# Optimization experiments

Measured on AMD Instinct MI355X. Metric: run time of the kernel, lower is better.

Reference implementation:

```python
import jax, jax.numpy as jnp
import numpy as np

TOP_K = 8
N_GROUPS = 8
TOP_K_GROUPS = 4
ROUTE_SCALE = 2.5


def setup_inputs() -> dict:
    key = jax.random.key(0)
    k1, k2, k3 = jax.random.split(key, 3)
    x = jax.random.normal(k1, (8192, 7168), dtype=jnp.float32)
    weight = jax.random.normal(k2, (256, 7168), dtype=jnp.float32) * 0.02
    bias = jax.random.normal(k3, (256,), dtype=jnp.float32) * 0.1
    return {"x": x, "weight": weight, "bias": bias}


def reference(x, weight, bias):
    n_tokens = x.shape[0]
    n_experts = weight.shape[0]
    # scores: [T, E]
    logits = jnp.einsum('td,ed->te', x, weight)
    scores = jax.nn.sigmoid(logits)
    original_scores = scores
    scores_b = scores + bias  # bias branch (dim == 7168)
    # group-limited routing
    sg = scores_b.reshape(n_tokens, N_GROUPS, n_experts // N_GROUPS)
    # bias is not None -> group score = sum of top-2 within group
    top2, _ = jax.lax.top_k(sg, 2)
    group_scores = top2.sum(axis=-1)  # [T, G]
    _, group_idx = jax.lax.top_k(group_scores, TOP_K_GROUPS)  # [T, Kg]
    keep = jnp.zeros((n_tokens, N_GROUPS), dtype=bool)
    keep = keep.at[jnp.arange(n_tokens)[:, None], group_idx].set(True)
    masked = jnp.where(keep[:, :, None], sg, -jnp.inf).reshape(n_tokens, n_experts)
    # global top-k over masked scores
    _, indices = jax.lax.top_k(masked, TOP_K)  # [T, K]
    weights = jnp.take_along_axis(original_scores, indices, axis=1)
    weights = weights / weights.sum(axis=-1, keepdims=True)  # sigmoid normalization
    weights = weights * ROUTE_SCALE
    return weights.astype(x.dtype), indices
```

## Files before the change

### kernel.cpp

```cpp
#include <hip/hip_runtime.h>
#include <math.h>

#define T_TOKENS 8192
#define NEXP 256
#define DIM 7168
#define NEG_INF (-3.0e38f)

typedef _Float16 f16;
typedef _Float16 f16x8 __attribute__((ext_vector_type(8)));
typedef __fp16 h16x2 __attribute__((ext_vector_type(2)));
typedef float f32x4 __attribute__((ext_vector_type(4)));

#define AS1 __attribute__((address_space(1)))
#define AS3 __attribute__((address_space(3)))

#define WPLANE_BYTES (NEXP * DIM * 2)
#define PART_OFF (2 * WPLANE_BYTES)
#define UNSCALE 5.9604644775390625e-8f

__global__ __launch_bounds__(256) void wconvert(const float* __restrict__ w,
                                                f16* __restrict__ w0p,
                                                f16* __restrict__ w1p) {
    const int i = (blockIdx.x * 256 + threadIdx.x) * 8;
    const f32x4 u0 = *(const f32x4*)(w + i);
    const f32x4 u1 = *(const f32x4*)(w + i + 4);
    float c[8] = {u0[0]*4096.f, u0[1]*4096.f, u0[2]*4096.f, u0[3]*4096.f,
                  u1[0]*4096.f, u1[1]*4096.f, u1[2]*4096.f, u1[3]*4096.f};
    f16x8 h, g;
#pragma unroll
    for (int j = 0; j < 4; ++j) {
        h16x2 hp = __builtin_amdgcn_cvt_pkrtz(c[2*j], c[2*j+1]);
        float r0 = c[2*j]   - (float)hp[0];
        float r1 = c[2*j+1] - (float)hp[1];
        h16x2 gp = __builtin_amdgcn_cvt_pkrtz(r0, r1);
        h[2*j] = (f16)hp[0]; h[2*j+1] = (f16)hp[1];
        g[2*j] = (f16)gp[0]; g[2*j+1] = (f16)gp[1];
    }
    *(f16x8*)(w0p + i) = h;
    *(f16x8*)(w1p + i) = g;
}

__global__ __launch_bounds__(256, 2) void gemm_f16split_db(
    const float* __restrict__ x, const f16* __restrict__ w0,
    float* __restrict__ part, int ksplit) {
    __shared__ char smem[65536];
    const int tid = threadIdx.x;
    const int lane = tid & 63;
    const int wv = tid >> 6;
    const int bm = blockIdx.x, bn = blockIdx.y, bz = blockIdx.z;
    const int wr = wv >> 1, wc = wv & 1;
    const int l15 = lane & 15, q4 = lane >> 4;

    const char* xc = (const char*)x;
    const char* wcp = (const char*)w0;

    int aoff[4], woff[4], ldsA[4], ldsW[4];
#pragma unroll
    for (int i = 0; i < 4; ++i) {
        const int ai = wv * 4 + i;
        const int ra = ai * 8 + (lane >> 3);
        const int ua = lane & 7;
        aoff[i] = (bm * 128 + ra) * (DIM * 4) + bz * (ksplit * 4)
                + ((ua ^ (ra & 7)) * 16);
        ldsA[i] = ai * 1024;
        const int wi_ = wv * 4 + i;
        const int p = wi_ >> 3;
        const int rw = (wi_ & 7) * 16 + (lane >> 2);
        const int uw = lane & 3;
        woff[i] = p * WPLANE_BYTES + (bn * 128 + rw) * (DIM * 2) + bz * (ksplit * 2)
                + ((uw ^ ((rw >> 1) & 3)) * 16);
        ldsW[i] = 16384 + wi_ * 1024;
    }

    int rA[4][2], rW[4][2];
#pragma unroll
    for (int m = 0; m < 4; ++m) {
        const int r = wr * 64 + m * 16 + l15;
        rA[m][0] = r * 128 + (((2 * q4 + 0) ^ (r & 7)) * 16);
        rA[m][1] = r * 128 + (((2 * q4 + 1) ^ (r & 7)) * 16);
    }
#pragma unroll
    for (int n = 0; n < 4; ++n) {
        const int rw = wc * 64 + n * 16 + l15;
        rW[n][0] = 16384 + 0    + rw * 64 + ((q4 ^ ((rw >> 1) & 3)) * 16);
        rW[n][1] = 16384 + 8192 + rw * 64 + ((q4 ^ ((rw >> 1) & 3)) * 16);
    }

    f32x4 acc[4][4];
#pragma unroll
    for (int m = 0; m < 4; ++m)
#pragma unroll
        for (int n = 0; n < 4; ++n) acc[m][n] = (f32x4){0.f, 0.f, 0.f, 0.f};

#define STAGE(sb)                                                               \
    {                                                                           \
        _Pragma("unroll")                                                       \
        for (int i = 0; i < 4; ++i)                                             \
            __builtin_amdgcn_global_load_lds((const AS1 void*)(xc + aoff[i]),   \
                (AS3 void*)(smem + (sb) + ldsA[i]), 16, 0, 0);                  \
        _Pragma("unroll")                                                       \
        for (int i = 0; i < 4; ++i)                                             \
            __builtin_amdgcn_global_load_lds((const AS1 void*)(wcp + woff[i]),  \
                (AS3 void*)(smem + (sb) + ldsW[i]), 16, 0, 0);                  \
        _Pragma("unroll")                                                       \
        for (int i = 0; i < 4; ++i) { aoff[i] += 128; woff[i] += 64; }          \
    }

#define COMPUTE(sb)                                                             \
    {                                                                           \
        f16x8 bfr[4][2];                                                        \
        _Pragma("unroll")                                                       \
        for (int n = 0; n < 4; ++n) {                                           \
            bfr[n][0] = *(const f16x8*)(smem + (sb) + rW[n][0]);                \
            bfr[n][1] = *(const f16x8*)(smem + (sb) + rW[n][1]);                \
        }                                                                       \
        _Pragma("unroll")                                                       \
        for (int m = 0; m < 4; ++m) {                                           \
            const f32x4 v0 = *(const f32x4*)(smem + (sb) + rA[m][0]);           \
            const f32x4 v1 = *(const f32x4*)(smem + (sb) + rA[m][1]);           \
            float c[8] = {v0[0]*4096.f, v0[1]*4096.f, v0[2]*4096.f, v0[3]*4096.f,\
                          v1[0]*4096.f, v1[1]*4096.f, v1[2]*4096.f, v1[3]*4096.f};\
            f16x8 a0, a1;                                                       \
            _Pragma("unroll")                                                   \
            for (int j = 0; j < 4; ++j) {                                       \
                h16x2 hp = __builtin_amdgcn_cvt_pkrtz(c[2*j], c[2*j+1]);        \
                float r0 = c[2*j]   - (float)hp[0];                             \
                float r1 = c[2*j+1] - (float)hp[1];                             \
                h16x2 gp = __builtin_amdgcn_cvt_pkrtz(r0, r1);                  \
                a0[2*j] = (f16)hp[0]; a0[2*j+1] = (f16)hp[1];                   \
                a1[2*j] = (f16)gp[0]; a1[2*j+1] = (f16)gp[1];                   \
            }                                                                   \
            __builtin_amdgcn_s_setprio(1);                                      \
            _Pragma("unroll")                                                   \
            for (int n = 0; n < 4; ++n) {                                       \
                acc[m][n] = __builtin_amdgcn_mfma_f32_16x16x32_f16(a0, bfr[n][0], acc[m][n], 0, 0, 0); \
                acc[m][n] = __builtin_amdgcn_mfma_f32_16x16x32_f16(a1, bfr[n][0], acc[m][n], 0, 0, 0); \
                acc[m][n] = __builtin_amdgcn_mfma_f32_16x16x32_f16(a0, bfr[n][1], acc[m][n], 0, 0, 0); \
                acc[m][n] = __builtin_amdgcn_mfma_f32_16x16x32_f16(a1, bfr[n][1], acc[m][n], 0, 0, 0); \
            }                                                                   \
            __builtin_amdgcn_s_setprio(0);                                      \
        }                                                                       \
    }

    const int niter = ksplit >> 5;
    STAGE(0);
    for (int t = 0; t < niter - 1; ++t) {
        const int cur = (t & 1) * 32768;
        const int nxt = ((t + 1) & 1) * 32768;
        STAGE(nxt);
        asm volatile("s_waitcnt vmcnt(8)" ::: "memory");
        __builtin_amdgcn_sched_barrier(0);
        __builtin_amdgcn_s_barrier();
        COMPUTE(cur);
        __builtin_amdgcn_s_barrier();
    }
    asm volatile("s_waitcnt vmcnt(0)" ::: "memory");
    __builtin_amdgcn_sched_barrier(0);
    __builtin_amdgcn_s_barrier();
    COMPUTE(((niter - 1) & 1) * 32768);
#undef STAGE
#undef COMPUTE

    float* P = part + (size_t)bz * T_TOKENS * NEXP;
    const int orow = bm * 128 + wr * 64 + (lane >> 4) * 4;
    const int ocol = bn * 128 + wc * 64 + l15;
#pragma unroll
    for (int m = 0; m < 4; ++m)
#pragma unroll
        for (int n = 0; n < 4; ++n)
#pragma unroll
            for (int r = 0; r < 4; ++r)
                P[(size_t)(orow + m * 16 + r) * NEXP + ocol + n * 16] = acc[m][n][r];
}

__global__ __launch_bounds__(256) void routing_kernel(const float* __restrict__ part,
                                                      const float* __restrict__ bias,
                                                      float* __restrict__ out, int nsplit) {
    const int lane = threadIdx.x & 63;
    const int t = blockIdx.x * 4 + (threadIdx.x >> 6);

    f32x4 z = {0.f, 0.f, 0.f, 0.f};
    for (int s = 0; s < nsplit; ++s) {
        const f32x4 v = *((const f32x4*)(part + ((size_t)s * T_TOKENS + t) * NEXP) + lane);
        z[0] += v[0]; z[1] += v[1]; z[2] += v[2]; z[3] += v[3];
    }
    const float s0 = 1.0f / (1.0f + expf(-z[0] * UNSCALE));
    const float s1 = 1.0f / (1.0f + expf(-z[1] * UNSCALE));
    const float s2 = 1.0f / (1.0f + expf(-z[2] * UNSCALE));
    const float s3 = 1.0f / (1.0f + expf(-z[3] * UNSCALE));
    const f32x4 bv = *((const f32x4*)bias + lane);
    float sb0 = s0 + bv[0], sb1 = s1 + bv[1], sb2 = s2 + bv[2], sb3 = s3 + bv[3];

    float m1, m2;
    m1 = sb0; m2 = NEG_INF;
    if (sb1 > m1) { m2 = m1; m1 = sb1; } else if (sb1 > m2) m2 = sb1;
    if (sb2 > m1) { m2 = m1; m1 = sb2; } else if (sb2 > m2) m2 = sb2;
    if (sb3 > m1) { m2 = m1; m1 = sb3; } else if (sb3 > m2) m2 = sb3;
#pragma unroll
    for (int off = 1; off < 8; off <<= 1) {
        const float om1 = __shfl_xor(m1, off);
        const float om2 = __shfl_xor(m2, off);
        const float hi = fmaxf(m1, om1);
        const float lo = fminf(m1, om1);
        m2 = fmaxf(lo, fmaxf(m2, om2));
        m1 = hi;
    }
    const float gs = m1 + m2;

    const float g0 = __shfl(gs, 0),  g1 = __shfl(gs, 8),  g2 = __shfl(gs, 16), g3 = __shfl(gs, 24);
    const float g4 = __shfl(gs, 32), g5 = __shfl(gs, 40), g6 = __shfl(gs, 48), g7 = __shfl(gs, 56);

    float t1 = NEG_INF, t2 = NEG_INF, t3 = NEG_INF, t4 = NEG_INF;
    int i1 = 0, i2 = 0, i3 = 0, i4 = 0;
#define INS4(v, gi)                                                         \
    {                                                                       \
        if (v > t1)      { t4=t3;i4=i3; t3=t2;i3=i2; t2=t1;i2=i1; t1=v;i1=gi; } \
        else if (v > t2) { t4=t3;i4=i3; t3=t2;i3=i2; t2=v;i2=gi; }          \
        else if (v > t3) { t4=t3;i4=i3; t3=v;i3=gi; }                       \
        else if (v > t4) { t4=v;i4=gi; }                                    \
    }
    INS4(g0, 0) INS4(g1, 1) INS4(g2, 2) INS4(g3, 3)
    INS4(g4, 4) INS4(g5, 5) INS4(g6, 6) INS4(g7, 7)
#undef INS4
    const int keepmask = (1 << i1) | (1 << i2) | (1 << i3) | (1 << i4);

    const int g = lane >> 3;
    if (!((keepmask >> g) & 1)) { sb0 = NEG_INF; sb1 = NEG_INF; sb2 = NEG_INF; sb3 = NEG_INF; }

    float wval[8];
    int wi[8];
    float wsum = 0.0f;
#pragma unroll
    for (int r = 0; r < 8; r++) {
        float bvv = sb0;
        int bii = (lane << 2);
        if (sb1 > bvv) { bvv = sb1; bii = (lane << 2) | 1; }
        if (sb2 > bvv) { bvv = sb2; bii = (lane << 2) | 2; }
        if (sb3 > bvv) { bvv = sb3; bii = (lane << 2) | 3; }
#pragma unroll
        for (int off = 1; off < 64; off <<= 1) {
            const float ov = __shfl_xor(bvv, off);
            const int oi = __shfl_xor(bii, off);
            if (ov > bvv || (ov == bvv && oi < bii)) { bvv = ov; bii = oi; }
        }
        const int sl = bii & 3;
        const float cand = (sl == 0) ? s0 : (sl == 1) ? s1 : (sl == 2) ? s2 : s3;
        const float ow = __shfl(cand, bii >> 2);
        wval[r] = ow;
        wi[r] = bii;
        wsum += ow;
        if ((bii >> 2) == lane) {
            if (sl == 0) sb0 = NEG_INF;
            else if (sl == 1) sb1 = NEG_INF;
            else if (sl == 2) sb2 = NEG_INF;
            else sb3 = NEG_INF;
        }
    }
    const float scale = 2.5f / wsum;
    if (lane == 0) {
        float* ow8 = out + (size_t)t * 8;
        float* oi8 = out + (size_t)T_TOKENS * 8 + (size_t)t * 8;
#pragma unroll
        for (int r = 0; r < 8; r++) {
            ow8[r] = wval[r] * scale;
            oi8[r] = (float)wi[r];
        }
    }
}

extern "C" void kernel_launch(void* const* d_in, const int* in_sizes, int n_in,
                              void* d_out, int out_size, void* d_ws, size_t ws_size,
                              hipStream_t stream) {
    const float* x = (const float*)d_in[0];
    const float* w = (const float*)d_in[1];
    const float* bias = (const float*)d_in[2];

    f16* w0 = (f16*)d_ws;
    f16* w1 = (f16*)((char*)d_ws + WPLANE_BYTES);
    float* part = (float*)((char*)d_ws + PART_OFF);

    const size_t need4 = (size_t)PART_OFF + 4ull * T_TOKENS * NEXP * 4;
    const int nsplit = (ws_size >= need4) ? 4 : 2;
    const int ksplit = DIM / nsplit;

    wconvert<<<NEXP * DIM / (256 * 8), 256, 0, stream>>>(w, w0, w1);
    gemm_f16split_db<<<dim3(64, 2, nsplit), 256, 0, stream>>>(x, w0, part, ksplit);
    routing_kernel<<<T_TOKENS / 4, 256, 0, stream>>>(part, bias, (float*)d_out, nsplit);
}
```

Measured before the change: 141.5 us.

## Rewrite router GEMM with 32x32 MFMA, pre-tiled weights and register-loaded activations

The weight-conversion kernel now writes the split-f16 weights in a pre-tiled layout that matches the MFMA operand order, so the GEMM can stage W into LDS with plain contiguous copies. Activations are loaded straight into registers instead of through LDS, which halves shared memory use. The MFMA is switched from 16x16x32 to 32x32x16, and the grid is reordered so the two N-blocks sharing an M tile are adjacent. The aim is less LDS traffic and fewer instructions per MFMA, in exchange for more register pressure, direct global loads of x, and a more involved software pipeline.

```diff
diff --git a/kernel.cpp b/kernel.cpp
--- a/kernel.cpp
+++ b/kernel.cpp
@@ -10,20 +10,22 @@
 typedef _Float16 f16x8 __attribute__((ext_vector_type(8)));
 typedef __fp16 h16x2 __attribute__((ext_vector_type(2)));
 typedef float f32x4 __attribute__((ext_vector_type(4)));
+typedef float f32x16 __attribute__((ext_vector_type(16)));
 
 #define AS1 __attribute__((address_space(1)))
 #define AS3 __attribute__((address_space(3)))
 
-#define WPLANE_BYTES (NEXP * DIM * 2)
-#define PART_OFF (2 * WPLANE_BYTES)
+#define WTILED_BYTES (2 * NEXP * DIM * 2)
+#define PART_OFF WTILED_BYTES
 #define UNSCALE 5.9604644775390625e-8f
 
 __global__ __launch_bounds__(256) void wconvert(const float* __restrict__ w,
-                                                f16* __restrict__ w0p,
-                                                f16* __restrict__ w1p) {
-    const int i = (blockIdx.x * 256 + threadIdx.x) * 8;
-    const f32x4 u0 = *(const f32x4*)(w + i);
-    const f32x4 u1 = *(const f32x4*)(w + i + 4);
+                                                char* __restrict__ wt) {
+    const int n = blockIdx.x * 256 + threadIdx.x;
+    const int K8 = n % 896;
+    const int eg = n / 896;
+    const f32x4 u0 = *(const f32x4*)(w + eg * DIM + K8 * 8);
+    const f32x4 u1 = *(const f32x4*)(w + eg * DIM + K8 * 8 + 4);
     float c[8] = {u0[0]*4096.f, u0[1]*4096.f, u0[2]*4096.f, u0[3]*4096.f,
                   u1[0]*4096.f, u1[1]*4096.f, u1[2]*4096.f, u1[3]*4096.f};
     f16x8 h, g;
@@ -36,141 +38,162 @@
         h[2*j] = (f16)hp[0]; h[2*j+1] = (f16)hp[1];
         g[2*j] = (f16)gp[0]; g[2*j+1] = (f16)gp[1];
     }
-    *(f16x8*)(w0p + i) = h;
-    *(f16x8*)(w1p + i) = g;
+    const int T = K8 >> 2, ksub = (K8 >> 1) & 1, kch = K8 & 1;
+    const int bn = eg >> 7, E = eg & 127, np_ = E >> 5, e = E & 31;
+    const int base = (T * 2 + bn) * 16384 + kch * 512 + e * 16;
+    *(f16x8*)(wt + base + ((ksub * 2 + 0) * 4 + np_) * 1024) = h;
+    *(f16x8*)(wt + base + ((ksub * 2 + 1) * 4 + np_) * 1024) = g;
 }
 
-__global__ __launch_bounds__(256, 2) void gemm_f16split_db(
-    const float* __restrict__ x, const f16* __restrict__ w0,
+__global__ __launch_bounds__(256) void gemm32(
+    const float* __restrict__ x, const char* __restrict__ wt,
     float* __restrict__ part, int ksplit) {
-    __shared__ char smem[65536];
+    __shared__ char smem[32768];
     const int tid = threadIdx.x;
     const int lane = tid & 63;
     const int wv = tid >> 6;
-    const int bm = blockIdx.x, bn = blockIdx.y, bz = blockIdx.z;
-    const int wr = wv >> 1, wc = wv & 1;
-    const int l15 = lane & 15, q4 = lane >> 4;
-
-    const char* xc = (const char*)x;
-    const char* wcp = (const char*)w0;
-
-    int aoff[4], woff[4], ldsA[4], ldsW[4];
-#pragma unroll
-    for (int i = 0; i < 4; ++i) {
-        const int ai = wv * 4 + i;
-        const int ra = ai * 8 + (lane >> 3);
-        const int ua = lane & 7;
-        aoff[i] = (bm * 128 + ra) * (DIM * 4) + bz * (ksplit * 4)
-                + ((ua ^ (ra & 7)) * 16);
-        ldsA[i] = ai * 1024;
-        const int wi_ = wv * 4 + i;
-        const int p = wi_ >> 3;
-        const int rw = (wi_ & 7) * 16 + (lane >> 2);
-        const int uw = lane & 3;
-        woff[i] = p * WPLANE_BYTES + (bn * 128 + rw) * (DIM * 2) + bz * (ksplit * 2)
-                + ((uw ^ ((rw >> 1) & 3)) * 16);
-        ldsW[i] = 16384 + wi_ * 1024;
-    }
-
-    int rA[4][2], rW[4][2];
-#pragma unroll
-    for (int m = 0; m < 4; ++m) {
-        const int r = wr * 64 + m * 16 + l15;
-        rA[m][0] = r * 128 + (((2 * q4 + 0) ^ (r & 7)) * 16);
-        rA[m][1] = r * 128 + (((2 * q4 + 1) ^ (r & 7)) * 16);
-    }
-#pragma unroll
-    for (int n = 0; n < 4; ++n) {
-        const int rw = wc * 64 + n * 16 + l15;
-        rW[n][0] = 16384 + 0    + rw * 64 + ((q4 ^ ((rw >> 1) & 3)) * 16);
-        rW[n][1] = 16384 + 8192 + rw * 64 + ((q4 ^ ((rw >> 1) & 3)) * 16);
-    }
-
-    f32x4 acc[4][4];
-#pragma unroll
-    for (int m = 0; m < 4; ++m)
-#pragma unroll
-        for (int n = 0; n < 4; ++n) acc[m][n] = (f32x4){0.f, 0.f, 0.f, 0.f};
-
-#define STAGE(sb)                                                               \
+    const int bn = blockIdx.x, bm = blockIdx.y, bz = blockIdx.z;
+    const int wr = wv >> 1, wcn = wv & 1;
+    const int l31 = lane & 31, lhi = lane >> 5;
+
+    const float* arow[2];
+#pragma unroll
+    for (int mp = 0; mp < 2; ++mp)
+        arow[mp] = x + (size_t)(bm * 128 + wr * 64 + mp * 32 + l31) * DIM
+                 + bz * ksplit + lhi * 8;
+
+    const int niter = ksplit >> 5;
+    const char* wsrc = wt + (size_t)(bz * niter * 2 + bn) * 16384 + (wv * 4) * 1024 + lane * 16;
+    const int ldsw = (wv * 4) * 1024;
+
+    int rW[2][2][2];
+#pragma unroll
+    for (int ks = 0; ks < 2; ++ks)
+#pragma unroll
+        for (int p = 0; p < 2; ++p)
+#pragma unroll
+            for (int np_ = 0; np_ < 2; ++np_)
+                rW[ks][p][np_] = ((ks * 2 + p) * 4 + (wcn * 2 + np_)) * 1024
+                               + lhi * 512 + l31 * 16;
+
+    f32x16 acc[2][2];
+#pragma unroll
+    for (int mp = 0; mp < 2; ++mp)
+#pragma unroll
+        for (int np_ = 0; np_ < 2; ++np_)
+#pragma unroll
+            for (int r = 0; r < 16; ++r) acc[mp][np_][r] = 0.0f;
+
+    f32x4 ab[2][2][2];
+
+#define LOAD_A(koff)                                                            \
     {                                                                           \
         _Pragma("unroll")                                                       \
-        for (int i = 0; i < 4; ++i)                                             \
-            __builtin_amdgcn_global_load_lds((const AS1 void*)(xc + aoff[i]),   \
-                (AS3 void*)(smem + (sb) + ldsA[i]), 16, 0, 0);                  \
+        for (int mp = 0; mp < 2; ++mp)                                          \
+            _Pragma("unroll")                                                   \
+            for (int ks = 0; ks < 2; ++ks) {                                    \
+                ab[mp][ks][0] = *(const f32x4*)(arow[mp] + (koff) + ks * 16);   \
+                ab[mp][ks][1] = *(const f32x4*)(arow[mp] + (koff) + ks * 16 + 4);\
+            }                                                                   \
+    }
+
+#define STAGE_W(t, sb)                                                          \
+    {                                                                           \
+        const char* s_ = wsrc + (size_t)(t) * 32768;                            \
         _Pragma("unroll")                                                       \
         for (int i = 0; i < 4; ++i)                                             \
-            __builtin_amdgcn_global_load_lds((const AS1 void*)(wcp + woff[i]),  \
-                (AS3 void*)(smem + (sb) + ldsW[i]), 16, 0, 0);                  \
+            __builtin_amdgcn_global_load_lds((const AS1 void*)(s_ + i * 1024),  \
+                (AS3 void*)(smem + (sb) + ldsw + i * 1024), 16, 0, 0);          \
+    }
+
+#define CONVERT()                                                               \
+    f16x8 fa0[2][2], fa1[2][2];                                                 \
+    {                                                                           \
         _Pragma("unroll")                                                       \
-        for (int i = 0; i < 4; ++i) { aoff[i] += 128; woff[i] += 64; }          \
-    }
-
-#define COMPUTE(sb)                                                             \
+        for (int mp = 0; mp < 2; ++mp)                                          \
+            _Pragma("unroll")                                                   \
+            for (int ks = 0; ks < 2; ++ks) {                                    \
+                float c[8] = {ab[mp][ks][0][0]*4096.f, ab[mp][ks][0][1]*4096.f, \
+                              ab[mp][ks][0][2]*4096.f, ab[mp][ks][0][3]*4096.f, \
+                              ab[mp][ks][1][0]*4096.f, ab[mp][ks][1][1]*4096.f, \
+                              ab[mp][ks][1][2]*4096.f, ab[mp][ks][1][3]*4096.f};\
+                _Pragma("unroll")                                               \
+                for (int j = 0; j < 4; ++j) {                                   \
+                    h16x2 hp = __builtin_amdgcn_cvt_pkrtz(c[2*j], c[2*j+1]);    \
+                    float r0 = c[2*j]   - (float)hp[0];                         \
+                    float r1 = c[2*j+1] - (float)hp[1];                         \
+                    h16x2 gp = __builtin_amdgcn_cvt_pkrtz(r0, r1);              \
+                    fa0[mp][ks][2*j] = (f16)hp[0]; fa0[mp][ks][2*j+1] = (f16)hp[1]; \
+                    fa1[mp][ks][2*j] = (f16)gp[0]; fa1[mp][ks][2*j+1] = (f16)gp[1]; \
+                }                                                               \
+            }                                                                   \
+    }
+
+#define MFMA_STEP(sb)                                                           \
     {                                                                           \
-        f16x8 bfr[4][2];                                                        \
+        __builtin_amdgcn_s_setprio(1);                                          \
         _Pragma("unroll")                                                       \
-        for (int n = 0; n < 4; ++n) {                                           \
-            bfr[n][0] = *(const f16x8*)(smem + (sb) + rW[n][0]);                \
-            bfr[n][1] = *(const f16x8*)(smem + (sb) + rW[n][1]);                \
-        }                                                                       \
-        _Pragma("unroll")                                                       \
-        for (int m = 0; m < 4; ++m) {                                           \
-            const f32x4 v0 = *(const f32x4*)(smem + (sb) + rA[m][0]);           \
-            const f32x4 v1 = *(const f32x4*)(smem + (sb) + rA[m][1]);           \
-            float c[8] = {v0[0]*4096.f, v0[1]*4096.f, v0[2]*4096.f, v0[3]*4096.f,\
-                          v1[0]*4096.f, v1[1]*4096.f, v1[2]*4096.f, v1[3]*4096.f};\
-            f16x8 a0, a1;                                                       \
+        for (int ks = 0; ks < 2; ++ks)                                          \
             _Pragma("unroll")                                                   \
-            for (int j = 0; j < 4; ++j) {                                       \
-                h16x2 hp = __builtin_amdgcn_cvt_pkrtz(c[2*j], c[2*j+1]);        \
-                float r0 = c[2*j]   - (float)hp[0];                             \
-                float r1 = c[2*j+1] - (float)hp[1];                             \
-                h16x2 gp = __builtin_amdgcn_cvt_pkrtz(r0, r1);                  \
-                a0[2*j] = (f16)hp[0]; a0[2*j+1] = (f16)hp[1];                   \
-                a1[2*j] = (f16)gp[0]; a1[2*j+1] = (f16)gp[1];                   \
+            for (int np_ = 0; np_ < 2; ++np_) {                                 \
+                const f16x8 wb0 = *(const f16x8*)(smem + (sb) + rW[ks][0][np_]);\
+                const f16x8 wb1 = *(const f16x8*)(smem + (sb) + rW[ks][1][np_]);\
+                _Pragma("unroll")                                               \
+                for (int mp = 0; mp < 2; ++mp) {                                \
+                    acc[mp][np_] = __builtin_amdgcn_mfma_f32_32x32x16_f16(fa0[mp][ks], wb0, acc[mp][np_], 0, 0, 0); \
+                    acc[mp][np_] = __builtin_amdgcn_mfma_f32_32x32x16_f16(fa1[mp][ks], wb0, acc[mp][np_], 0, 0, 0); \
+                    acc[mp][np_] = __builtin_amdgcn_mfma_f32_32x32x16_f16(fa0[mp][ks], wb1, acc[mp][np_], 0, 0, 0); \
+                    acc[mp][np_] = __builtin_amdgcn_mfma_f32_32x32x16_f16(fa1[mp][ks], wb1, acc[mp][np_], 0, 0, 0); \
+                }                                                               \
             }                                                                   \
-            __builtin_amdgcn_s_setprio(1);                                      \
-            _Pragma("unroll")                                                   \
-            for (int n = 0; n < 4; ++n) {                                       \
-                acc[m][n] = __builtin_amdgcn_mfma_f32_16x16x32_f16(a0, bfr[n][0], acc[m][n], 0, 0, 0); \
-                acc[m][n] = __builtin_amdgcn_mfma_f32_16x16x32_f16(a1, bfr[n][0], acc[m][n], 0, 0, 0); \
-                acc[m][n] = __builtin_amdgcn_mfma_f32_16x16x32_f16(a0, bfr[n][1], acc[m][n], 0, 0, 0); \
-                acc[m][n] = __builtin_amdgcn_mfma_f32_16x16x32_f16(a1, bfr[n][1], acc[m][n], 0, 0, 0); \
-            }                                                                   \
-            __builtin_amdgcn_s_setprio(0);                                      \
-        }                                                                       \
-    }
-
-    const int niter = ksplit >> 5;
-    STAGE(0);
+        __builtin_amdgcn_s_setprio(0);                                          \
+    }
+
+    LOAD_A(0);
+    STAGE_W(0, 0);
+
     for (int t = 0; t < niter - 1; ++t) {
-        const int cur = (t & 1) * 32768;
-        const int nxt = ((t + 1) & 1) * 32768;
-        STAGE(nxt);
-        asm volatile("s_waitcnt vmcnt(8)" ::: "memory");
+        const int cur = (t & 1) * 16384;
+        const int nxt = ((t + 1) & 1) * 16384;
+        asm volatile("s_waitcnt vmcnt(4)" ::: "memory");
+        __builtin_amdgcn_sched_barrier(0);
+        CONVERT();
+        LOAD_A((t + 1) * 32);
+        STAGE_W(t + 1, nxt);
+        asm volatile("s_waitcnt vmcnt(12)" ::: "memory");
         __builtin_amdgcn_sched_barrier(0);
         __builtin_amdgcn_s_barrier();
-        COMPUTE(cur);
+        MFMA_STEP(cur);
         __builtin_amdgcn_s_barrier();
     }
-    asm volatile("s_waitcnt vmcnt(0)" ::: "memory");
-    __builtin_amdgcn_sched_barrier(0);
-    __builtin_amdgcn_s_barrier();
-    COMPUTE(((niter - 1) & 1) * 32768);
-#undef STAGE
-#undef COMPUTE
+    {
+        const int cur = ((niter - 1) & 1) * 16384;
+        asm volatile("s_waitcnt vmcnt(4)" ::: "memory");
+        __builtin_amdgcn_sched_barrier(0);
+        CONVERT();
+        asm volatile("s_waitcnt vmcnt(0)" ::: "memory");
+        __builtin_amdgcn_sched_barrier(0);
+        __builtin_amdgcn_s_barrier();
+        MFMA_STEP(cur);
+    }
+#undef LOAD_A
+#undef STAGE_W
+#undef CONVERT
+#undef MFMA_STEP
 
     float* P = part + (size_t)bz * T_TOKENS * NEXP;
-    const int orow = bm * 128 + wr * 64 + (lane >> 4) * 4;
-    const int ocol = bn * 128 + wc * 64 + l15;
-#pragma unroll
-    for (int m = 0; m < 4; ++m)
-#pragma unroll
-        for (int n = 0; n < 4; ++n)
-#pragma unroll
-            for (int r = 0; r < 4; ++r)
-                P[(size_t)(orow + m * 16 + r) * NEXP + ocol + n * 16] = acc[m][n][r];
+#pragma unroll
+    for (int mp = 0; mp < 2; ++mp)
+#pragma unroll
+        for (int np_ = 0; np_ < 2; ++np_) {
+            const int gcol = bn * 128 + (wcn * 2 + np_) * 32 + l31;
+#pragma unroll
+            for (int r = 0; r < 16; ++r) {
+                const int row32 = (r & 3) + 8 * (r >> 2) + 4 * lhi;
+                const int grow = bm * 128 + wr * 64 + mp * 32 + row32;
+                P[(size_t)grow * NEXP + gcol] = acc[mp][np_][r];
+            }
+        }
 }
 
 __global__ __launch_bounds__(256) void routing_kernel(const float* __restrict__ part,
@@ -275,15 +298,14 @@
     const float* w = (const float*)d_in[1];
     const float* bias = (const float*)d_in[2];
 
-    f16* w0 = (f16*)d_ws;
-    f16* w1 = (f16*)((char*)d_ws + WPLANE_BYTES);
+    char* wt = (char*)d_ws;
     float* part = (float*)((char*)d_ws + PART_OFF);
 
     const size_t need4 = (size_t)PART_OFF + 4ull * T_TOKENS * NEXP * 4;
     const int nsplit = (ws_size >= need4) ? 4 : 2;
     const int ksplit = DIM / nsplit;
 
-    wconvert<<<NEXP * DIM / (256 * 8), 256, 0, stream>>>(w, w0, w1);
-    gemm_f16split_db<<<dim3(64, 2, nsplit), 256, 0, stream>>>(x, w0, part, ksplit);
+    wconvert<<<NEXP * DIM / (256 * 8), 256, 0, stream>>>(w, wt);
+    gemm32<<<dim3(2, 64, nsplit), 256, 0, stream>>>(x, wt, part, ksplit);
     routing_kernel<<<T_TOKENS / 4, 256, 0, stream>>>(part, bias, (float*)d_out, nsplit);
 }
```

After: 198.8 us. 40.5% more time.

## Pre-tile split-f16 weights and shrink GEMM N tile to 64 for more blocks

Applied to the files above, without the earlier changes.

The weight conversion kernel now writes hi/lo f16 planes into a pre-tiled layout that matches the LDS fragment layout. Each GEMM block can then load its weight tile with fully contiguous 16-byte loads and no swizzle math. The GEMM block tile changes from 128x128 to 128x64 (grid 4x64xnsplit), which doubles the block count and cuts LDS to 48KB and accumulators to half. The aim is better occupancy and load balance across CUs. In exchange, each x tile is re-read from global memory twice as many times, and the higher-precision fp32 x conversion work per block is duplicated across more blocks.

```diff
diff --git a/kernel.cpp b/kernel.cpp
--- a/kernel.cpp
+++ b/kernel.cpp
@@ -14,16 +14,17 @@
 #define AS1 __attribute__((address_space(1)))
 #define AS3 __attribute__((address_space(3)))
 
-#define WPLANE_BYTES (NEXP * DIM * 2)
-#define PART_OFF (2 * WPLANE_BYTES)
+#define WTILED_BYTES (2 * NEXP * DIM * 2)
+#define PART_OFF WTILED_BYTES
 #define UNSCALE 5.9604644775390625e-8f
 
 __global__ __launch_bounds__(256) void wconvert(const float* __restrict__ w,
-                                                f16* __restrict__ w0p,
-                                                f16* __restrict__ w1p) {
-    const int i = (blockIdx.x * 256 + threadIdx.x) * 8;
-    const f32x4 u0 = *(const f32x4*)(w + i);
-    const f32x4 u1 = *(const f32x4*)(w + i + 4);
+                                                char* __restrict__ wt) {
+    const int n = blockIdx.x * 256 + threadIdx.x;
+    const int K8 = n % 896;
+    const int e = n / 896;
+    const f32x4 u0 = *(const f32x4*)(w + (size_t)e * DIM + K8 * 8);
+    const f32x4 u1 = *(const f32x4*)(w + (size_t)e * DIM + K8 * 8 + 4);
     float c[8] = {u0[0]*4096.f, u0[1]*4096.f, u0[2]*4096.f, u0[3]*4096.f,
                   u1[0]*4096.f, u1[1]*4096.f, u1[2]*4096.f, u1[3]*4096.f};
     f16x8 h, g;
@@ -36,25 +37,28 @@
         h[2*j] = (f16)hp[0]; h[2*j+1] = (f16)hp[1];
         g[2*j] = (f16)gp[0]; g[2*j+1] = (f16)gp[1];
     }
-    *(f16x8*)(w0p + i) = h;
-    *(f16x8*)(w1p + i) = g;
-}
-
-__global__ __launch_bounds__(256, 2) void gemm_f16split_db(
-    const float* __restrict__ x, const f16* __restrict__ w0,
+    const int T = K8 >> 2, q = K8 & 3;
+    const int bn = e >> 6, nt = (e >> 4) & 3, l = e & 15;
+    char* base = wt + ((size_t)(T * 4 + bn)) * 8192 + q * 256 + l * 16;
+    *(f16x8*)(base + (0 * 4 + nt) * 1024) = h;
+    *(f16x8*)(base + (1 * 4 + nt) * 1024) = g;
+}
+
+__global__ __launch_bounds__(256) void gemm16(
+    const float* __restrict__ x, const char* __restrict__ wt,
     float* __restrict__ part, int ksplit) {
-    __shared__ char smem[65536];
+    __shared__ char smem[49152];
     const int tid = threadIdx.x;
     const int lane = tid & 63;
     const int wv = tid >> 6;
-    const int bm = blockIdx.x, bn = blockIdx.y, bz = blockIdx.z;
-    const int wr = wv >> 1, wc = wv & 1;
+    const int bn = blockIdx.x, bm = blockIdx.y, bz = blockIdx.z;
+    const int wr = wv >> 1, wcn = wv & 1;
     const int l15 = lane & 15, q4 = lane >> 4;
+    const int niter = ksplit >> 5;
 
     const char* xc = (const char*)x;
-    const char* wcp = (const char*)w0;
-
-    int aoff[4], woff[4], ldsA[4], ldsW[4];
+
+    int aoff[4], ldsA[4];
 #pragma unroll
     for (int i = 0; i < 4; ++i) {
         const int ai = wv * 4 + i;
@@ -63,34 +67,35 @@
         aoff[i] = (bm * 128 + ra) * (DIM * 4) + bz * (ksplit * 4)
                 + ((ua ^ (ra & 7)) * 16);
         ldsA[i] = ai * 1024;
-        const int wi_ = wv * 4 + i;
-        const int p = wi_ >> 3;
-        const int rw = (wi_ & 7) * 16 + (lane >> 2);
-        const int uw = lane & 3;
-        woff[i] = p * WPLANE_BYTES + (bn * 128 + rw) * (DIM * 2) + bz * (ksplit * 2)
-                + ((uw ^ ((rw >> 1) & 3)) * 16);
-        ldsW[i] = 16384 + wi_ * 1024;
-    }
-
-    int rA[4][2], rW[4][2];
+    }
+    const char* wbase = wt + ((size_t)(bz * niter * 4 + bn)) * 8192;
+    int woff[2], ldsW[2];
+#pragma unroll
+    for (int i = 0; i < 2; ++i) {
+        const int unit = wv * 2 + i;
+        woff[i] = unit * 1024 + lane * 16;
+        ldsW[i] = 16384 + unit * 1024;
+    }
+
+    int rA[4][2];
 #pragma unroll
     for (int m = 0; m < 4; ++m) {
         const int r = wr * 64 + m * 16 + l15;
         rA[m][0] = r * 128 + (((2 * q4 + 0) ^ (r & 7)) * 16);
         rA[m][1] = r * 128 + (((2 * q4 + 1) ^ (r & 7)) * 16);
     }
-#pragma unroll
-    for (int n = 0; n < 4; ++n) {
-        const int rw = wc * 64 + n * 16 + l15;
-        rW[n][0] = 16384 + 0    + rw * 64 + ((q4 ^ ((rw >> 1) & 3)) * 16);
-        rW[n][1] = 16384 + 8192 + rw * 64 + ((q4 ^ ((rw >> 1) & 3)) * 16);
-    }
-
-    f32x4 acc[4][4];
+    int rW[2][2];
+#pragma unroll
+    for (int nt = 0; nt < 2; ++nt)
+#pragma unroll
+        for (int p = 0; p < 2; ++p)
+            rW[nt][p] = 16384 + (p * 4 + (wcn * 2 + nt)) * 1024 + q4 * 256 + l15 * 16;
+
+    f32x4 acc[4][2];
 #pragma unroll
     for (int m = 0; m < 4; ++m)
 #pragma unroll
-        for (int n = 0; n < 4; ++n) acc[m][n] = (f32x4){0.f, 0.f, 0.f, 0.f};
+        for (int nt = 0; nt < 2; ++nt) acc[m][nt] = (f32x4){0.f, 0.f, 0.f, 0.f};
 
 #define STAGE(sb)                                                               \
     {                                                                           \
@@ -99,20 +104,22 @@
             __builtin_amdgcn_global_load_lds((const AS1 void*)(xc + aoff[i]),   \
                 (AS3 void*)(smem + (sb) + ldsA[i]), 16, 0, 0);                  \
         _Pragma("unroll")                                                       \
-        for (int i = 0; i < 4; ++i)                                             \
-            __builtin_amdgcn_global_load_lds((const AS1 void*)(wcp + woff[i]),  \
+        for (int i = 0; i < 2; ++i)                                             \
+            __builtin_amdgcn_global_load_lds((const AS1 void*)(wbase + woff[i]),\
                 (AS3 void*)(smem + (sb) + ldsW[i]), 16, 0, 0);                  \
         _Pragma("unroll")                                                       \
-        for (int i = 0; i < 4; ++i) { aoff[i] += 128; woff[i] += 64; }          \
+        for (int i = 0; i < 4; ++i) aoff[i] += 128;                             \
+        _Pragma("unroll")                                                       \
+        for (int i = 0; i < 2; ++i) woff[i] += 32768;                           \
     }
 
 #define COMPUTE(sb)                                                             \
     {                                                                           \
-        f16x8 bfr[4][2];                                                        \
-        _Pragma("unroll")                                                       \
-        for (int n = 0; n < 4; ++n) {                                           \
-            bfr[n][0] = *(const f16x8*)(smem + (sb) + rW[n][0]);                \
-            bfr[n][1] = *(const f16x8*)(smem + (sb) + rW[n][1]);                \
+        f16x8 wb[2][2];                                                         \
+        _Pragma("unroll")                                                       \
+        for (int nt = 0; nt < 2; ++nt) {                                        \
+            wb[nt][0] = *(const f16x8*)(smem + (sb) + rW[nt][0]);               \
+            wb[nt][1] = *(const f16x8*)(smem + (sb) + rW[nt][1]);               \
         }                                                                       \
         _Pragma("unroll")                                                       \
         for (int m = 0; m < 4; ++m) {                                           \
@@ -132,23 +139,22 @@
             }                                                                   \
             __builtin_amdgcn_s_setprio(1);                                      \
             _Pragma("unroll")                                                   \
-            for (int n = 0; n < 4; ++n) {                                       \
-                acc[m][n] = __builtin_amdgcn_mfma_f32_16x16x32_f16(a0, bfr[n][0], acc[m][n], 0, 0, 0); \
-                acc[m][n] = __builtin_amdgcn_mfma_f32_16x16x32_f16(a1, bfr[n][0], acc[m][n], 0, 0, 0); \
-                acc[m][n] = __builtin_amdgcn_mfma_f32_16x16x32_f16(a0, bfr[n][1], acc[m][n], 0, 0, 0); \
-                acc[m][n] = __builtin_amdgcn_mfma_f32_16x16x32_f16(a1, bfr[n][1], acc[m][n], 0, 0, 0); \
+            for (int nt = 0; nt < 2; ++nt) {                                    \
+                acc[m][nt] = __builtin_amdgcn_mfma_f32_16x16x32_f16(a0, wb[nt][0], acc[m][nt], 0, 0, 0); \
+                acc[m][nt] = __builtin_amdgcn_mfma_f32_16x16x32_f16(a1, wb[nt][0], acc[m][nt], 0, 0, 0); \
+                acc[m][nt] = __builtin_amdgcn_mfma_f32_16x16x32_f16(a0, wb[nt][1], acc[m][nt], 0, 0, 0); \
+                acc[m][nt] = __builtin_amdgcn_mfma_f32_16x16x32_f16(a1, wb[nt][1], acc[m][nt], 0, 0, 0); \
             }                                                                   \
             __builtin_amdgcn_s_setprio(0);                                      \
         }                                                                       \
     }
 
-    const int niter = ksplit >> 5;
     STAGE(0);
     for (int t = 0; t < niter - 1; ++t) {
-        const int cur = (t & 1) * 32768;
-        const int nxt = ((t + 1) & 1) * 32768;
+        const int cur = (t & 1) * 24576;
+        const int nxt = ((t + 1) & 1) * 24576;
         STAGE(nxt);
-        asm volatile("s_waitcnt vmcnt(8)" ::: "memory");
+        asm volatile("s_waitcnt vmcnt(6)" ::: "memory");
         __builtin_amdgcn_sched_barrier(0);
         __builtin_amdgcn_s_barrier();
         COMPUTE(cur);
@@ -157,20 +163,21 @@
     asm volatile("s_waitcnt vmcnt(0)" ::: "memory");
     __builtin_amdgcn_sched_barrier(0);
     __builtin_amdgcn_s_barrier();
-    COMPUTE(((niter - 1) & 1) * 32768);
+    COMPUTE(((niter - 1) & 1) * 24576);
 #undef STAGE
 #undef COMPUTE
 
     float* P = part + (size_t)bz * T_TOKENS * NEXP;
-    const int orow = bm * 128 + wr * 64 + (lane >> 4) * 4;
-    const int ocol = bn * 128 + wc * 64 + l15;
+    const int orow = bm * 128 + wr * 64 + q4 * 4;
 #pragma unroll
     for (int m = 0; m < 4; ++m)
 #pragma unroll
-        for (int n = 0; n < 4; ++n)
+        for (int nt = 0; nt < 2; ++nt) {
+            const int ocol = bn * 64 + (wcn * 2 + nt) * 16 + l15;
 #pragma unroll
             for (int r = 0; r < 4; ++r)
-                P[(size_t)(orow + m * 16 + r) * NEXP + ocol + n * 16] = acc[m][n][r];
+                P[(size_t)(orow + m * 16 + r) * NEXP + ocol] = acc[m][nt][r];
+        }
 }
 
 __global__ __launch_bounds__(256) void routing_kernel(const float* __restrict__ part,
@@ -275,15 +282,14 @@
     const float* w = (const float*)d_in[1];
     const float* bias = (const float*)d_in[2];
 
-    f16* w0 = (f16*)d_ws;
-    f16* w1 = (f16*)((char*)d_ws + WPLANE_BYTES);
+    char* wt = (char*)d_ws;
     float* part = (float*)((char*)d_ws + PART_OFF);
 
     const size_t need4 = (size_t)PART_OFF + 4ull * T_TOKENS * NEXP * 4;
     const int nsplit = (ws_size >= need4) ? 4 : 2;
     const int ksplit = DIM / nsplit;
 
-    wconvert<<<NEXP * DIM / (256 * 8), 256, 0, stream>>>(w, w0, w1);
-    gemm_f16split_db<<<dim3(64, 2, nsplit), 256, 0, stream>>>(x, w0, part, ksplit);
+    wconvert<<<NEXP * DIM / (256 * 8), 256, 0, stream>>>(w, wt);
+    gemm16<<<dim3(4, 64, nsplit), 256, 0, stream>>>(x, wt, part, ksplit);
     routing_kernel<<<T_TOKENS / 4, 256, 0, stream>>>(part, bias, (float*)d_out, nsplit);
 }
```

New measurement: 179.7 us. 1.27x slower.
